# Optimization experiments

Hardware: AMD Instinct MI355X
Metric: run time of the kernel (lower is better)

## Reference

```python
import jax, jax.numpy as jnp
import numpy as np

B = 8192          # batch rows
C_IN = 4096       # total input channels
G = 8             # number of clusters
CG = C_IN // G    # channels per cluster (arrangement.shape[0])
J = 512           # j_rank per cluster (output width per cluster)


def setup_inputs() -> dict:
    key = jax.random.key(0)
    kx, kp, kw, kb = jax.random.split(key, 4)
    x = jax.random.normal(kx, (B, C_IN), dtype=jnp.float32)
    # arrangements: a random permutation of all input channels split into G groups,
    # mimicking channel-clustering assignments (each channel used exactly once)
    perm = jax.random.permutation(kp, C_IN)
    arrangements = perm.reshape(G, CG).astype(jnp.int64)
    # per-group nn.Linear weights: torch layout (out_features, in_features)
    weights = jax.random.normal(kw, (G, J, CG), dtype=jnp.float32) * (1.0 / np.sqrt(CG))
    bias = jax.random.normal(kb, (G, J), dtype=jnp.float32) * 0.02
    return {"x": x, "arrangements": arrangements, "weights": weights, "bias": bias}


def reference(x, arrangements, weights, bias):
    # Gather each cluster's channels: x[:, arrangements] -> [B, G, CG]
    xg = jnp.take(x, arrangements, axis=1)
    # Per-group linear (torch Linear: y = x @ W.T + b), batched over groups,
    # then concat along feature dim -> [B, G*J]
    out = jnp.einsum('bgc,gjc->bgj', xg, weights) + bias[None, :, :]
    return out.reshape(x.shape[0], -1)
```

## Files before the change

### kernel.cpp

```cpp
#include <hip/hip_runtime.h>
#include <hip/hip_bf16.h>

#define B_ROWS 8192
#define C_IN   4096
#define G_GRP  8
#define CG     512
#define J_RANK 512

#define BM 128
#define BN 256
#define BK 32
#define NKT (CG / BK)

#define RPB    8
#define PERM_BLOCKS (B_ROWS / RPB)
#define CONV_BLOCKS 128

typedef __attribute__((ext_vector_type(8))) short bf16x8;
typedef __attribute__((ext_vector_type(4))) float f32x4;
typedef __attribute__((ext_vector_type(8))) unsigned short u16x8;

struct ushort4v { unsigned short x, y, z, w; };

__device__ __forceinline__ unsigned short f2bf(float f) {
    unsigned int u = __float_as_uint(f);
    unsigned int r = (u + 0x7FFFu + ((u >> 16) & 1u)) >> 16;
    return (unsigned short)r;
}

__global__ __launch_bounds__(256) void permute_x_kernel(
    const float* __restrict__ x, const int* __restrict__ arr,
    unsigned short* __restrict__ xp,
    const float* __restrict__ w, unsigned short* __restrict__ wb) {
    const int tid = threadIdx.x;

    if (blockIdx.x >= PERM_BLOCKS) {
        const int cb = blockIdx.x - PERM_BLOCKS;
#pragma unroll
        for (int t = 0; t < 16; ++t) {
            int i = cb * 4096 + t * 256 + tid;
            float4 v = ((const float4*)w)[i];
            ushort4v o;
            o.x = f2bf(v.x); o.y = f2bf(v.y); o.z = f2bf(v.z); o.w = f2bf(v.w);
            ((ushort4v*)wb)[i] = o;
        }
        return;
    }

    __shared__ float buf[3][C_IN];
    const int row0 = blockIdx.x * RPB;

    const bool is64 = (arr[1] == 0 && arr[3] == 0 && arr[5] == 0 && arr[7] == 0);

    int sidx[16];
#pragma unroll
    for (int pass = 0; pass < 2; ++pass)
#pragma unroll
        for (int k = 0; k < 8; ++k) {
            int p = pass * 2048 + tid * 8 + k;
            sidx[pass * 8 + k] = is64 ? arr[2 * p] : arr[p];
        }

#define PSTAGE(bufi, r)                                                      \
    do {                                                                     \
        const float* src_ = x + (size_t)(row0 + (r)) * C_IN;                 \
        _Pragma("unroll")                                                    \
        for (int i_ = 0; i_ < 4; ++i_) {                                     \
            int c_ = i_ * 256 + tid;                                         \
            __builtin_amdgcn_global_load_lds(                                \
                (const __attribute__((address_space(1))) unsigned int*)      \
                    (src_ + c_ * 4),                                         \
                (__attribute__((address_space(3))) unsigned int*)            \
                    (&buf[bufi][0] + c_ * 4),                                \
                16, 0, 0);                                                   \
        }                                                                    \
    } while (0)

    PSTAGE(0, 0);
    PSTAGE(1, 1);

#pragma unroll
    for (int r = 0; r < RPB; ++r) {
        if (r == 0)            asm volatile("s_waitcnt vmcnt(4)" ::: "memory");
        else if (r == 1)       asm volatile("s_waitcnt vmcnt(6)" ::: "memory");
        else if (r == RPB - 1) asm volatile("s_waitcnt vmcnt(4)" ::: "memory");
        else                   asm volatile("s_waitcnt vmcnt(8)" ::: "memory");
        __builtin_amdgcn_s_barrier();
        __builtin_amdgcn_sched_barrier(0);

        if (r + 2 < RPB) PSTAGE((r + 2) % 3, r + 2);

        const int bi = r % 3;
        unsigned short* orow = xp + (size_t)(row0 + r) * C_IN;
#pragma unroll
        for (int pass = 0; pass < 2; ++pass) {
            u16x8 o;
#pragma unroll
            for (int k = 0; k < 8; ++k)
                o[k] = f2bf(buf[bi][sidx[pass * 8 + k]]);
            *(u16x8*)(orow + pass * 2048 + tid * 8) = o;
        }
        __builtin_amdgcn_sched_barrier(0);
    }
#undef PSTAGE
}

__global__ __launch_bounds__(512, 4) void gemm_kernel(
    const unsigned short* __restrict__ Xp,
    const unsigned short* __restrict__ Wb,
    const float* __restrict__ bias,
    float* __restrict__ out) {
    __shared__ unsigned short ldsA[3][BM * BK];
    __shared__ unsigned short ldsB[2][BN * BK];

    const int tid = threadIdx.x;
    const int g   = blockIdx.x & 7;
    const int idx = blockIdx.x >> 3;
    const int mt  = idx >> 1;
    const int nt  = idx & 1;

    const int l   = tid & 63;
    const int wv  = tid >> 6;
    const int wr  = wv >> 2;
    const int wc  = wv & 3;
    const int lr  = l & 15;
    const int lkq = l >> 4;

    const unsigned short* Ab = Xp + (size_t)(mt * BM) * C_IN + g * CG;
    const unsigned short* Bb = Wb + (size_t)g * J_RANK * CG + (size_t)(nt * BN) * CG;

    f32x4 acc[4][4];
#pragma unroll
    for (int m = 0; m < 4; ++m)
#pragma unroll
        for (int n = 0; n < 4; ++n) acc[m][n] = (f32x4){0.f, 0.f, 0.f, 0.f};

    const int coff = (lkq ^ ((lr >> 2) & 3)) * 8;

#define STAGE_A(kt_)                                                          \
    do { const int p_ = (kt_) % 3;                                            \
        int c_ = tid;                                                         \
        int rl_ = c_ >> 2, gc_ = (c_ & 3) ^ ((rl_ >> 2) & 3);                 \
        __builtin_amdgcn_global_load_lds(                                     \
            (const __attribute__((address_space(1))) unsigned int*)           \
                (Ab + (size_t)rl_ * C_IN + (kt_) * BK + gc_ * 8),             \
            (__attribute__((address_space(3))) unsigned int*)                 \
                (&ldsA[p_][0] + c_ * 8),                                      \
            16, 0, 0);                                                        \
    } while (0)

#define STAGE_B(kt_)                                                          \
    do { const int p_ = (kt_) & 1;                                            \
        _Pragma("unroll")                                                     \
        for (int i_ = 0; i_ < 2; ++i_) {                                      \
            int c_ = i_ * 512 + tid;                                          \
            int rl_ = c_ >> 2, gc_ = (c_ & 3) ^ ((rl_ >> 2) & 3);             \
            __builtin_amdgcn_global_load_lds(                                 \
                (const __attribute__((address_space(1))) unsigned int*)       \
                    (Bb + (size_t)rl_ * CG + (kt_) * BK + gc_ * 8),           \
                (__attribute__((address_space(3))) unsigned int*)             \
                    (&ldsB[p_][0] + c_ * 8),                                  \
                16, 0, 0);                                                    \
        }                                                                     \
    } while (0)

#define LDA(m_) (*(const bf16x8*)&ldsA[bufA][(wr * 64 + (m_) * 16 + lr) * BK + coff])
#define LDB(n_) (*(const bf16x8*)&ldsB[bufB][(wc * 64 + (n_) * 16 + lr) * BK + coff])

#define PHASE_TAIL()                                                          \
    __builtin_amdgcn_s_barrier();                                             \
    asm volatile("s_waitcnt lgkmcnt(0)" ::: "memory");                        \
    __builtin_amdgcn_sched_barrier(0);                                        \
    __builtin_amdgcn_s_setprio(1)

#define PHASE_END()                                                           \
    __builtin_amdgcn_s_setprio(0);                                            \
    __builtin_amdgcn_s_barrier()

    STAGE_A(0); STAGE_B(0);
    STAGE_A(1); STAGE_B(1);
    asm volatile("s_waitcnt vmcnt(3)" ::: "memory");
    __builtin_amdgcn_s_barrier();

    bf16x8 bfr[4], af[2];

    for (int kt = 0; kt < NKT; ++kt) {
        const int bufA = kt % 3;
        const int bufB = kt & 1;

#pragma unroll
        for (int n = 0; n < 4; ++n) bfr[n] = LDB(n);
        af[0] = LDA(0); af[1] = LDA(1);
        if (kt + 2 < NKT) STAGE_A(kt + 2);
        PHASE_TAIL();
#pragma unroll
        for (int mm = 0; mm < 2; ++mm)
#pragma unroll
            for (int n = 0; n < 4; ++n)
                acc[mm][n] = __builtin_amdgcn_mfma_f32_16x16x32_bf16(
                    af[mm], bfr[n], acc[mm][n], 0, 0, 0);
        PHASE_END();

        af[0] = LDA(2); af[1] = LDA(3);
        if (kt + 2 < NKT) STAGE_B(kt + 2);
        if (kt <= NKT - 3)      asm volatile("s_waitcnt vmcnt(3)" ::: "memory");
        else if (kt == NKT - 2) asm volatile("s_waitcnt vmcnt(0)" ::: "memory");
        PHASE_TAIL();
#pragma unroll
        for (int mm = 0; mm < 2; ++mm)
#pragma unroll
            for (int n = 0; n < 4; ++n)
                acc[2 + mm][n] = __builtin_amdgcn_mfma_f32_16x16x32_bf16(
                    af[mm], bfr[n], acc[2 + mm][n], 0, 0, 0);
        PHASE_END();
    }
#undef STAGE_A
#undef STAGE_B
#undef LDA
#undef LDB
#undef PHASE_TAIL
#undef PHASE_END

    const int r0 = mt * BM + wr * 64 + (lkq << 2);
    const int cbase = nt * BN + wc * 64 + lr;
#pragma unroll
    for (int n = 0; n < 4; ++n) {
        int col = cbase + n * 16;
        float bv = bias[g * J_RANK + col];
#pragma unroll
        for (int m = 0; m < 4; ++m) {
            int row = r0 + m * 16;
            float* op = out + (size_t)row * C_IN + g * J_RANK + col;
#pragma unroll
            for (int r = 0; r < 4; ++r)
                op[(size_t)r * C_IN] = acc[m][n][r] + bv;
        }
    }
}

extern "C" void kernel_launch(void* const* d_in, const int* in_sizes, int n_in,
                              void* d_out, int out_size, void* d_ws, size_t ws_size,
                              hipStream_t stream) {
    const float* x    = (const float*)d_in[0];
    const int*   arr  = (const int*)d_in[1];
    const float* w    = (const float*)d_in[2];
    const float* bias = (const float*)d_in[3];
    float* out = (float*)d_out;

    unsigned short* xp = (unsigned short*)d_ws;
    unsigned short* wb = xp + (size_t)B_ROWS * C_IN;

    hipLaunchKernelGGL(permute_x_kernel, dim3(PERM_BLOCKS + CONV_BLOCKS),
                       dim3(256), 0, stream, x, arr, xp, w, wb);
    hipLaunchKernelGGL(gemm_kernel,
                       dim3(G_GRP * (B_ROWS / BM) * (J_RANK / BN)), dim3(512),
                       0, stream, xp, wb, bias, out);
}
```

Baseline: 102.2 us.

## Merge permute and GEMM into one kernel and overlap halves across launches

Combines the permute/convert kernel and the GEMM kernel into one kernel that dispatches on block index. The work is split into three launches: permute the first half of rows plus convert the weights, then run the GEMM on the first half while permuting the second half, then run the GEMM on the second half. This is meant to overlap the memory-bound permutation with the compute-bound GEMM. The permute path now runs with 512 threads and uses the GEMM's larger shared-memory footprint, which may lower permute occupancy, and the change adds a third launch.

Result: slower. 110.0 us (+7.6%).

```diff
diff --git a/kernel.cpp b/kernel.cpp
--- a/kernel.cpp
+++ b/kernel.cpp
@@ -12,9 +12,10 @@
 #define BK 32
 #define NKT (CG / BK)
 
-#define RPB    8
-#define PERM_BLOCKS (B_ROWS / RPB)
-#define CONV_BLOCKS 128
+#define RPB 8
+#define HALF_ROWS 4096
+#define HALF_PERM_BLOCKS (HALF_ROWS / RPB)
+#define CONV_BLOCKS 64
 
 typedef __attribute__((ext_vector_type(8))) short bf16x8;
 typedef __attribute__((ext_vector_type(4))) float f32x4;
@@ -28,17 +29,21 @@
     return (unsigned short)r;
 }
 
-__global__ __launch_bounds__(256) void permute_x_kernel(
+__global__ __launch_bounds__(512, 4) void mega_kernel(
     const float* __restrict__ x, const int* __restrict__ arr,
     unsigned short* __restrict__ xp,
-    const float* __restrict__ w, unsigned short* __restrict__ wb) {
+    const float* __restrict__ w, unsigned short* __restrict__ wb,
+    const float* __restrict__ bias, float* __restrict__ out,
+    int n_gemm, int gemm_mt_base, int n_perm, int perm_row_base) {
+    __shared__ __align__(16) unsigned char smem[57344];
     const int tid = threadIdx.x;
-
-    if (blockIdx.x >= PERM_BLOCKS) {
-        const int cb = blockIdx.x - PERM_BLOCKS;
+    const int bid = blockIdx.x;
+
+    if (bid >= n_gemm + n_perm) {
+        const int cb = bid - n_gemm - n_perm;
 #pragma unroll
         for (int t = 0; t < 16; ++t) {
-            int i = cb * 4096 + t * 256 + tid;
+            int i = cb * 8192 + t * 512 + tid;
             float4 v = ((const float4*)w)[i];
             ushort4v o;
             o.x = f2bf(v.x); o.y = f2bf(v.y); o.z = f2bf(v.z); o.w = f2bf(v.w);
@@ -47,76 +52,65 @@
         return;
     }
 
-    __shared__ float buf[3][C_IN];
-    const int row0 = blockIdx.x * RPB;
-
-    const bool is64 = (arr[1] == 0 && arr[3] == 0 && arr[5] == 0 && arr[7] == 0);
-
-    int sidx[16];
-#pragma unroll
-    for (int pass = 0; pass < 2; ++pass)
+    if (bid >= n_gemm) {
+        float* buf = (float*)smem;
+        const int pb   = bid - n_gemm;
+        const int row0 = perm_row_base + pb * RPB;
+
+        const bool is64 = (arr[1] == 0 && arr[3] == 0 && arr[5] == 0 && arr[7] == 0);
+        int sidx[8];
 #pragma unroll
         for (int k = 0; k < 8; ++k) {
-            int p = pass * 2048 + tid * 8 + k;
-            sidx[pass * 8 + k] = is64 ? arr[2 * p] : arr[p];
-        }
-
-#define PSTAGE(bufi, r)                                                      \
+            int p = tid * 8 + k;
+            sidx[k] = is64 ? arr[2 * p] : arr[p];
+        }
+
+#define PSTAGE(s_, r_)                                                       \
     do {                                                                     \
-        const float* src_ = x + (size_t)(row0 + (r)) * C_IN;                 \
+        const float* src_ = x + (size_t)(row0 + (r_)) * C_IN;                \
         _Pragma("unroll")                                                    \
-        for (int i_ = 0; i_ < 4; ++i_) {                                     \
-            int c_ = i_ * 256 + tid;                                         \
+        for (int i_ = 0; i_ < 2; ++i_) {                                     \
+            int c_ = i_ * 2048 + tid * 4;                                    \
             __builtin_amdgcn_global_load_lds(                                \
                 (const __attribute__((address_space(1))) unsigned int*)      \
-                    (src_ + c_ * 4),                                         \
+                    (src_ + c_),                                             \
                 (__attribute__((address_space(3))) unsigned int*)            \
-                    (&buf[bufi][0] + c_ * 4),                                \
+                    (buf + (s_) * C_IN + c_),                                \
                 16, 0, 0);                                                   \
         }                                                                    \
     } while (0)
 
-    PSTAGE(0, 0);
-    PSTAGE(1, 1);
-
-#pragma unroll
-    for (int r = 0; r < RPB; ++r) {
-        if (r == 0)            asm volatile("s_waitcnt vmcnt(4)" ::: "memory");
-        else if (r == 1)       asm volatile("s_waitcnt vmcnt(6)" ::: "memory");
-        else if (r == RPB - 1) asm volatile("s_waitcnt vmcnt(4)" ::: "memory");
-        else                   asm volatile("s_waitcnt vmcnt(8)" ::: "memory");
-        __builtin_amdgcn_s_barrier();
-        __builtin_amdgcn_sched_barrier(0);
-
-        if (r + 2 < RPB) PSTAGE((r + 2) % 3, r + 2);
-
-        const int bi = r % 3;
-        unsigned short* orow = xp + (size_t)(row0 + r) * C_IN;
-#pragma unroll
-        for (int pass = 0; pass < 2; ++pass) {
+        PSTAGE(0, 0);
+        PSTAGE(1, 1);
+
+#pragma unroll
+        for (int r = 0; r < RPB; ++r) {
+            if (r == 0)            asm volatile("s_waitcnt vmcnt(2)" ::: "memory");
+            else if (r == 1)       asm volatile("s_waitcnt vmcnt(3)" ::: "memory");
+            else if (r == RPB - 1) asm volatile("s_waitcnt vmcnt(2)" ::: "memory");
+            else                   asm volatile("s_waitcnt vmcnt(4)" ::: "memory");
+            __builtin_amdgcn_s_barrier();
+            __builtin_amdgcn_sched_barrier(0);
+
+            if (r + 2 < RPB) PSTAGE((r + 2) % 3, r + 2);
+
+            const float* bi = buf + (r % 3) * C_IN;
             u16x8 o;
 #pragma unroll
-            for (int k = 0; k < 8; ++k)
-                o[k] = f2bf(buf[bi][sidx[pass * 8 + k]]);
-            *(u16x8*)(orow + pass * 2048 + tid * 8) = o;
-        }
-        __builtin_amdgcn_sched_barrier(0);
-    }
+            for (int k = 0; k < 8; ++k) o[k] = f2bf(bi[sidx[k]]);
+            *(u16x8*)(xp + (size_t)(row0 + r) * C_IN + tid * 8) = o;
+            __builtin_amdgcn_sched_barrier(0);
+        }
 #undef PSTAGE
-}
-
-__global__ __launch_bounds__(512, 4) void gemm_kernel(
-    const unsigned short* __restrict__ Xp,
-    const unsigned short* __restrict__ Wb,
-    const float* __restrict__ bias,
-    float* __restrict__ out) {
-    __shared__ unsigned short ldsA[3][BM * BK];
-    __shared__ unsigned short ldsB[2][BN * BK];
-
-    const int tid = threadIdx.x;
-    const int g   = blockIdx.x & 7;
-    const int idx = blockIdx.x >> 3;
-    const int mt  = idx >> 1;
+        return;
+    }
+
+    unsigned short* ldsA = (unsigned short*)smem;
+    unsigned short* ldsB = (unsigned short*)(smem + 3 * BM * BK * 2);
+
+    const int g   = bid & 7;
+    const int idx = bid >> 3;
+    const int mt  = gemm_mt_base + (idx >> 1);
     const int nt  = idx & 1;
 
     const int l   = tid & 63;
@@ -126,8 +120,8 @@
     const int lr  = l & 15;
     const int lkq = l >> 4;
 
-    const unsigned short* Ab = Xp + (size_t)(mt * BM) * C_IN + g * CG;
-    const unsigned short* Bb = Wb + (size_t)g * J_RANK * CG + (size_t)(nt * BN) * CG;
+    const unsigned short* Ab = xp + (size_t)(mt * BM) * C_IN + g * CG;
+    const unsigned short* Bb = wb + (size_t)g * J_RANK * CG + (size_t)(nt * BN) * CG;
 
     f32x4 acc[4][4];
 #pragma unroll
@@ -145,7 +139,7 @@
             (const __attribute__((address_space(1))) unsigned int*)           \
                 (Ab + (size_t)rl_ * C_IN + (kt_) * BK + gc_ * 8),             \
             (__attribute__((address_space(3))) unsigned int*)                 \
-                (&ldsA[p_][0] + c_ * 8),                                      \
+                (ldsA + p_ * (BM * BK) + c_ * 8),                             \
             16, 0, 0);                                                        \
     } while (0)
 
@@ -159,13 +153,13 @@
                 (const __attribute__((address_space(1))) unsigned int*)       \
                     (Bb + (size_t)rl_ * CG + (kt_) * BK + gc_ * 8),           \
                 (__attribute__((address_space(3))) unsigned int*)             \
-                    (&ldsB[p_][0] + c_ * 8),                                  \
+                    (ldsB + p_ * (BN * BK) + c_ * 8),                         \
                 16, 0, 0);                                                    \
         }                                                                     \
     } while (0)
 
-#define LDA(m_) (*(const bf16x8*)&ldsA[bufA][(wr * 64 + (m_) * 16 + lr) * BK + coff])
-#define LDB(n_) (*(const bf16x8*)&ldsB[bufB][(wc * 64 + (n_) * 16 + lr) * BK + coff])
+#define LDA(m_) (*(const bf16x8*)&ldsA[bufA * (BM * BK) + (wr * 64 + (m_) * 16 + lr) * BK + coff])
+#define LDB(n_) (*(const bf16x8*)&ldsB[bufB * (BN * BK) + (wc * 64 + (n_) * 16 + lr) * BK + coff])
 
 #define PHASE_TAIL()                                                          \
     __builtin_amdgcn_s_barrier();                                             \
@@ -250,9 +244,13 @@
     unsigned short* xp = (unsigned short*)d_ws;
     unsigned short* wb = xp + (size_t)B_ROWS * C_IN;
 
-    hipLaunchKernelGGL(permute_x_kernel, dim3(PERM_BLOCKS + CONV_BLOCKS),
-                       dim3(256), 0, stream, x, arr, xp, w, wb);
-    hipLaunchKernelGGL(gemm_kernel,
-                       dim3(G_GRP * (B_ROWS / BM) * (J_RANK / BN)), dim3(512),
-                       0, stream, xp, wb, bias, out);
+    hipLaunchKernelGGL(mega_kernel, dim3(HALF_PERM_BLOCKS + CONV_BLOCKS), dim3(512),
+                       0, stream, x, arr, xp, w, wb, bias, out,
+                       0, 0, HALF_PERM_BLOCKS, 0);
+    hipLaunchKernelGGL(mega_kernel, dim3(512 + HALF_PERM_BLOCKS), dim3(512),
+                       0, stream, x, arr, xp, w, wb, bias, out,
+                       512, 0, HALF_PERM_BLOCKS, HALF_ROWS);
+    hipLaunchKernelGGL(mega_kernel, dim3(512), dim3(512),
+                       0, stream, x, arr, xp, w, wb, bias, out,
+                       512, 32, 0, 0);
 }
```
